# Kernel tuning notes

Hardware: AMD Instinct MI355X
Metric: run time of the kernel (lower is better)

## Reference

```python
import jax, jax.numpy as jnp
import numpy as np

N = 50000      # nodes
E = 800000     # edges (avg degree 16)
D_IN = 64
H = 128        # capacity
LAT = 64       # latent_dim
LN_EPS = 1e-5


def setup_inputs() -> dict:
    key = jax.random.key(0)
    ks = jax.random.split(key, 16)
    inp = {}
    inp["x"] = jax.random.normal(ks[0], (N, D_IN), dtype=jnp.float32)
    inp["edge_index"] = jax.random.randint(ks[1], (2, E), 0, N)
    dims = [(D_IN, H), (H, H), (H, LAT)]
    ki = 2
    for t in ("m", "v"):  # mu tower / logvar tower
        for i, (di, do) in enumerate(dims):
            s = 1.0 / np.sqrt(di)
            inp[f"{t}Wl{i}"] = jax.random.normal(ks[ki], (do, di), jnp.float32) * s; ki += 1
            inp[f"{t}bl{i}"] = jnp.zeros((do,), jnp.float32)
            inp[f"{t}Wr{i}"] = jax.random.normal(ks[ki], (do, di), jnp.float32) * s; ki += 1
            if i < 2:  # LayerNorm on hidden layers only
                inp[f"{t}g{i}"] = jnp.ones((do,), jnp.float32)
                inp[f"{t}b{i}"] = jnp.zeros((do,), jnp.float32)
    return inp


def _ln(h, g, b):
    m = h.mean(-1, keepdims=True)
    v = h.var(-1, keepdims=True)
    return (h - m) * jax.lax.rsqrt(v + LN_EPS) * g + b


def _sage(h, src, dst, inv_deg, Wl, bl, Wr):
    # mean neighbor aggregation: scatter-add messages h[src] into dst, divide by degree
    agg = jax.ops.segment_sum(h[src], dst, num_segments=N) * inv_deg  # [N, d_in]
    # PyG SAGEConv: lin_l(agg) [with bias] + lin_r(h_root) [no bias]
    return agg @ Wl.T + bl + h @ Wr.T


def _tower(x, src, dst, inv_deg, layers):
    h = x
    L = len(layers)
    for i, lay in enumerate(layers):
        h = _sage(h, src, dst, inv_deg, lay[0], lay[1], lay[2])
        if i < L - 1:
            h = jax.nn.relu(_ln(h, lay[3], lay[4]))
    return h


def reference(x, edge_index,
              mWl0, mbl0, mWr0, mg0, mb0,
              mWl1, mbl1, mWr1, mg1, mb1,
              mWl2, mbl2, mWr2,
              vWl0, vbl0, vWr0, vg0, vb0,
              vWl1, vbl1, vWr1, vg1, vb1,
              vWl2, vbl2, vWr2):
    src, dst = edge_index[0], edge_index[1]
    deg = jax.ops.segment_sum(jnp.ones((E,), x.dtype), dst, num_segments=N)
    inv_deg = (1.0 / jnp.maximum(deg, 1.0))[:, None]
    mu_layers = [(mWl0, mbl0, mWr0, mg0, mb0),
                 (mWl1, mbl1, mWr1, mg1, mb1),
                 (mWl2, mbl2, mWr2)]
    lv_layers = [(vWl0, vbl0, vWr0, vg0, vb0),
                 (vWl1, vbl1, vWr1, vg1, vb1),
                 (vWl2, vbl2, vWr2)]
    mu = _tower(x, src, dst, inv_deg, mu_layers)
    lv = _tower(x, src, dst, inv_deg, lv_layers)
    return mu, lv
```

## Files before the change

### kernel.cpp

```cpp
#include <hip/hip_runtime.h>

#define NN 50000
#define NE 800000
#define MPAD 50048
#define NBK 196
#define FB 98
#define CH4 2048
#define EB4 200000
#define STAGE_CAP 6144

typedef __attribute__((ext_vector_type(8))) short short8;
typedef __attribute__((ext_vector_type(4))) float f32x4;
typedef uint __attribute__((ext_vector_type(4))) uintx4;
typedef uint __attribute__((ext_vector_type(2))) uintx2;
typedef int __attribute__((ext_vector_type(2))) intx2;

__device__ __forceinline__ ushort f2b(float f) {
    uint u = __builtin_bit_cast(uint, f);
    uint r = (u + 0x7fffu + ((u >> 16) & 1u)) >> 16;
    return (ushort)r;
}
__device__ __forceinline__ uint pk2(float a, float b) {
    return (uint)f2b(a) | ((uint)f2b(b) << 16);
}
__device__ __forceinline__ float blo(uint u) { return __builtin_bit_cast(float, u << 16); }
__device__ __forceinline__ float bhi(uint u) { return __builtin_bit_cast(float, u & 0xffff0000u); }

__device__ __forceinline__ void acc8(float* a, uintx4 u) {
    a[0] += blo(u[0]); a[1] += bhi(u[0]);
    a[2] += blo(u[1]); a[3] += bhi(u[1]);
    a[4] += blo(u[2]); a[5] += bhi(u[2]);
    a[6] += blo(u[3]); a[7] += bhi(u[3]);
}
__device__ __forceinline__ void acc4(float* a, uintx2 u) {
    a[0] += blo(u[0]); a[1] += bhi(u[0]);
    a[2] += blo(u[1]); a[3] += bhi(u[1]);
}


struct W2Args {
    const float* srcA[8];
    const float* srcB[8];
    ushort* dst[8];
};


struct PrepArgs {
    const float* x; ushort* xb;
    W2Args w;
    const int* edst; int* bhist;
};

__global__ __launch_bounds__(256) void k_prep(PrepArgs a) {
    __shared__ int h[NBK];
    int b = blockIdx.x;
    int t = threadIdx.x;
    if (b < FB) {
        for (int i = t; i < NBK; i += 256) h[i] = 0;
        __syncthreads();
        int i1 = min((b + 1) * CH4, EB4);
        for (int i = b * CH4 + t; i < i1; i += 256) {
            int4 d = ((const int4*)a.edst)[i];
            atomicAdd(&h[d.x >> 8], 1);
            atomicAdd(&h[d.y >> 8], 1);
            atomicAdd(&h[d.z >> 8], 1);
            atomicAdd(&h[d.w >> 8], 1);
        }
        __syncthreads();
        for (int i = t; i < NBK; i += 256) a.bhist[b * NBK + i] = h[i];
    } else if (b < FB + 512) {
        const int offT[8]   = {0, 16384, 49152, 57344, 65536, 81920, 114688, 122880};
        const int splitT[8] = {64, 128, 128, 0, 64, 128, 128, 0};
        const int logKKT[8] = {7, 8, 7, 7, 7, 8, 7, 7};
        const int ntT[8]    = {8, 8, 4, 4, 8, 8, 4, 4};
        int idx = (b - FB) * 256 + t;
        if (idx >= 131072) return;
        int L = 0;
#pragma unroll
        for (int i = 1; i < 8; ++i) if (idx >= offT[i]) L = i;
        int j = idx - offT[L];
        int lk = logKKT[L];
        int KK = 1 << lk;
        int n = j >> lk;
        int c = j & (KK - 1);
        int split = splitT[L];
        float v = (c < split) ? a.w.srcA[L][n * split + c]
                              : a.w.srcB[L][n * (KK - split) + (c - split)];
        int ks = c >> 5, kseg = (c >> 3) & 3, jj = c & 7;
        int nt = n >> 4, r15 = n & 15;
        int lane = (kseg << 4) | r15;
        int foff = ((ks * ntT[L] + nt) << 9) + (lane << 3) + jj;
        a.w.dst[L][foff] = f2b(v);
    } else {
        int i = (b - FB - 512) * 256 + t;
        if (i < NN * 32) {
            float2 v = *(const float2*)(a.x + (size_t)i * 2);
            *(uint*)(a.xb + (size_t)i * 2) = pk2(v.x, v.y);
        }
    }
}


__global__ __launch_bounds__(256) void k_fscan(const int* __restrict__ bhist,
                                               int* __restrict__ pairRel,
                                               int* __restrict__ bbase) {
    __shared__ int tot[256];
    int b = threadIdx.x;
    int run = 0;
    if (b < NBK) {
        for (int blk = 0; blk < FB; ++blk) {
            int v = bhist[blk * NBK + b];
            pairRel[blk * NBK + b] = run;
            run += v;
        }
    }
    tot[b] = (b < NBK) ? run : 0;
    __syncthreads();
    for (int off = 1; off < 256; off <<= 1) {
        int t = (b >= off) ? tot[b - off] : 0;
        __syncthreads();
        tot[b] += t;
        __syncthreads();
    }
    if (b < NBK) bbase[b] = tot[b] - run;
    if (b == NBK - 1) bbase[NBK] = tot[b];
}

__global__ __launch_bounds__(256) void k_f2(const int* __restrict__ src, const int* __restrict__ dst,
                                            const int* __restrict__ pairRel,
                                            const int* __restrict__ bbase, intx2* __restrict__ pairs) {
    __shared__ int cur[NBK];
    for (int i = threadIdx.x; i < NBK; i += 256)
        cur[i] = bbase[i] + pairRel[blockIdx.x * NBK + i];
    __syncthreads();
    int i1 = min((int)(blockIdx.x + 1) * CH4, EB4);
    for (int i = blockIdx.x * CH4 + threadIdx.x; i < i1; i += 256) {
        int4 s = ((const int4*)src)[i];
        int4 d = ((const int4*)dst)[i];
        int p0 = atomicAdd(&cur[d.x >> 8], 1);
        int p1 = atomicAdd(&cur[d.y >> 8], 1);
        int p2 = atomicAdd(&cur[d.z >> 8], 1);
        int p3 = atomicAdd(&cur[d.w >> 8], 1);
        __builtin_nontemporal_store((intx2){s.x, d.x}, &pairs[p0]);
        __builtin_nontemporal_store((intx2){s.y, d.y}, &pairs[p1]);
        __builtin_nontemporal_store((intx2){s.z, d.z}, &pairs[p2]);
        __builtin_nontemporal_store((intx2){s.w, d.w}, &pairs[p3]);
    }
}

__global__ __launch_bounds__(256) void k_f3(const intx2* __restrict__ pairs,
                                            const int* __restrict__ bbase,
                                            int* __restrict__ row_start,
                                            float* __restrict__ inv_deg,
                                            int* __restrict__ col) {
    __shared__ int ndeg[256];
    __shared__ int noff[256];
    __shared__ int stage[STAGE_CAP];
    int b = blockIdx.x;
    int base = bbase[b], end = bbase[b + 1];
    int nbase = b << 8;
    int t = threadIdx.x;
    ndeg[t] = 0;
    __syncthreads();
    for (int p = base + t; p < end; p += 256) {
        intx2 pr = pairs[p];
        atomicAdd(&ndeg[pr[1] - nbase], 1);
    }
    __syncthreads();
    int d = ndeg[t];
    noff[t] = d;
    __syncthreads();
    for (int off = 1; off < 256; off <<= 1) {
        int v = (t >= off) ? noff[t - off] : 0;
        __syncthreads();
        noff[t] += v;
        __syncthreads();
    }
    int excl = noff[t] - d;
    int node = nbase + t;
    if (node < NN) {
        row_start[node] = base + excl;
        inv_deg[node] = 1.0f / (float)(d > 1 ? d : 1);
    }
    if (b == 0 && t == 0) row_start[NN] = NE;
    __syncthreads();
    noff[t] = excl;
    __syncthreads();
    int cnt = end - base;
    for (int p = base + t; p < end; p += 256) {
        intx2 pr = pairs[p];
        int pos = atomicAdd(&noff[pr[1] - nbase], 1);
        if (pos < STAGE_CAP) stage[pos] = pr[0];
        else col[base + pos] = pr[0];
    }
    __syncthreads();
    int lim = cnt < STAGE_CAP ? cnt : STAGE_CAP;
    for (int i = t; i < lim; i += 256) col[base + i] = stage[i];
}


template <int D>
__global__ __launch_bounds__(256) void k_agg(
    const ushort* __restrict__ h,
    const int* __restrict__ row_start, const int* __restrict__ col,
    const float* __restrict__ inv_deg, ushort* __restrict__ o) {
    constexpr int LPN = (D == 256) ? 32 : 16;
    int gid = blockIdx.x * 256 + threadIdx.x;
    int node = gid / LPN;
    int li = gid & (LPN - 1);
    if (node >= NN) return;
    int s = row_start[node], e = row_start[node + 1];
    float sc = inv_deg[node];
    if (D == 64) {
        const ushort* hb = h + li * 4;
        float a[4] = {0, 0, 0, 0};
        int p = s;
        for (; p + 15 < e; p += 16) {
            int cc[16];
#pragma unroll
            for (int j = 0; j < 16; ++j) cc[j] = __builtin_nontemporal_load(col + p + j);
#pragma unroll
            for (int j = 0; j < 16; ++j) acc4(a, *(const uintx2*)(hb + (size_t)cc[j] * 64));
        }
        for (; p + 3 < e; p += 4) {
            int cc[4];
#pragma unroll
            for (int j = 0; j < 4; ++j) cc[j] = __builtin_nontemporal_load(col + p + j);
#pragma unroll
            for (int j = 0; j < 4; ++j) acc4(a, *(const uintx2*)(hb + (size_t)cc[j] * 64));
        }
        for (; p < e; ++p) acc4(a, *(const uintx2*)(hb + (size_t)col[p] * 64));
        uintx2 r;
        r[0] = pk2(a[0] * sc, a[1] * sc);
        r[1] = pk2(a[2] * sc, a[3] * sc);
        __builtin_nontemporal_store(r, (uintx2*)(o + (size_t)node * 64 + li * 4));
    } else {
        const ushort* hb = h + li * 8;
        float a[8] = {0, 0, 0, 0, 0, 0, 0, 0};
        int p = s;
        for (; p + 15 < e; p += 16) {
            int cc[16];
#pragma unroll
            for (int j = 0; j < 16; ++j) cc[j] = __builtin_nontemporal_load(col + p + j);
#pragma unroll
            for (int j = 0; j < 16; ++j) acc8(a, *(const uintx4*)(hb + (size_t)cc[j] * D));
        }
        for (; p + 3 < e; p += 4) {
            int cc[4];
#pragma unroll
            for (int j = 0; j < 4; ++j) cc[j] = __builtin_nontemporal_load(col + p + j);
#pragma unroll
            for (int j = 0; j < 4; ++j) acc8(a, *(const uintx4*)(hb + (size_t)cc[j] * D));
        }
        for (; p < e; ++p) acc8(a, *(const uintx4*)(hb + (size_t)col[p] * D));
        uintx4 r;
        r[0] = pk2(a[0] * sc, a[1] * sc);
        r[1] = pk2(a[2] * sc, a[3] * sc);
        r[2] = pk2(a[4] * sc, a[5] * sc);
        r[3] = pk2(a[6] * sc, a[7] * sc);
        __builtin_nontemporal_store(r, (uintx4*)(o + (size_t)node * D + li * 8));
    }
}


struct GArgs {
    const ushort *A1, *A2, *Wm, *Wv;
    const float *blm, *blv, *gm, *gv, *bbm, *bbv;
    void* out;
};

template <int KH, int NOUT, bool DO_LN, bool DUAL, int ASTR, int AOFFM, int OSTR, int OOFFM>
__global__ __launch_bounds__(256, 2) void k_gemm(GArgs a) {
    constexpr int NT = NOUT / 16;
    constexpr int NK = KH / 16;
    constexpr int TW = DUAL ? 2 : 1;
    constexpr int WCH = NOUT * KH * 4 / 16;
    __shared__ uint4 wlds[TW * WCH];

    int tid = threadIdx.x;
    int lane = tid & 63, wid = tid >> 6;
    int tow = DUAL ? 0 : blockIdx.y;
    int aoff = tow * AOFFM;

    {
        const uint4* w0 = (const uint4*)(tow ? a.Wv : a.Wm);
        for (int i = tid; i < WCH; i += 256) wlds[i] = w0[i];
        if (DUAL) {
            const uint4* w1 = (const uint4*)a.Wv;
            for (int i = tid; i < WCH; i += 256) wlds[WCH + i] = w1[i];
        }
    }

    int r15 = lane & 15, kseg = lane >> 4;
    int m0 = blockIdx.x * 128 + wid * 32;
    size_t ar0 = (size_t)(m0 + r15);
    size_t ar1 = (size_t)(m0 + 16 + r15);

    short8 af[2][NK];
#pragma unroll
    for (int ks = 0; ks < NK; ++ks) {
        int kc = ks * 32 + kseg * 8;
        af[0][ks] = (kc < KH) ? *(const short8*)(a.A1 + ar0 * ASTR + aoff + kc)
                              : *(const short8*)(a.A2 + ar0 * ASTR + aoff + (kc - KH));
        af[1][ks] = (kc < KH) ? *(const short8*)(a.A1 + ar1 * ASTR + aoff + kc)
                              : *(const short8*)(a.A2 + ar1 * ASTR + aoff + (kc - KH));
    }
    __syncthreads();

    f32x4 acc[TW][2][NT];
#pragma unroll
    for (int tt = 0; tt < TW; ++tt)
#pragma unroll
        for (int t = 0; t < 2; ++t)
#pragma unroll
            for (int nt = 0; nt < NT; ++nt) acc[tt][t][nt] = (f32x4){0.f, 0.f, 0.f, 0.f};

#pragma unroll
    for (int ks = 0; ks < NK; ++ks) {
#pragma unroll
        for (int nt = 0; nt < NT; ++nt) {
#pragma unroll
            for (int tt = 0; tt < TW; ++tt) {
                short8 w = *(const short8*)&wlds[tt * WCH + (ks * NT + nt) * 64 + lane];
                acc[tt][0][nt] = __builtin_amdgcn_mfma_f32_16x16x32_bf16(af[0][ks], w, acc[tt][0][nt], 0, 0, 0);
                acc[tt][1][nt] = __builtin_amdgcn_mfma_f32_16x16x32_bf16(af[1][ks], w, acc[tt][1][nt], 0, 0, 0);
            }
        }
    }

#pragma unroll
    for (int tt = 0; tt < TW; ++tt) {
        int tsel = DUAL ? tt : tow;
        int ooff = tsel * OOFFM;
        const float* bl = tsel ? a.blv : a.blm;
#pragma unroll
        for (int nt = 0; nt < NT; ++nt) {
            float bb = bl[nt * 16 + r15];
#pragma unroll
            for (int t = 0; t < 2; ++t)
#pragma unroll
                for (int r = 0; r < 4; ++r) acc[tt][t][nt][r] += bb;
        }
        if (DO_LN) {
            const float* g = tsel ? a.gv : a.gm;
            const float* b = tsel ? a.bbv : a.bbm;
#pragma unroll
            for (int t = 0; t < 2; ++t) {
                float s[4] = {0, 0, 0, 0}, q[4] = {0, 0, 0, 0};
#pragma unroll
                for (int nt = 0; nt < NT; ++nt)
#pragma unroll
                    for (int r = 0; r < 4; ++r) { float v = acc[tt][t][nt][r]; s[r] += v; q[r] += v * v; }
#pragma unroll
                for (int off = 1; off < 16; off <<= 1)
#pragma unroll
                    for (int r = 0; r < 4; ++r) { s[r] += __shfl_xor(s[r], off); q[r] += __shfl_xor(q[r], off); }
                float mean[4], rstd[4];
#pragma unroll
                for (int r = 0; r < 4; ++r) {
                    mean[r] = s[r] * (1.0f / NOUT);
                    float var = q[r] * (1.0f / NOUT) - mean[r] * mean[r];
                    rstd[r] = rsqrtf(var + 1e-5f);
                }
                ushort* out = (ushort*)a.out;
#pragma unroll
                for (int nt = 0; nt < NT; ++nt) {
                    int n = nt * 16 + r15;
                    float gg = g[n], bb = b[n];
#pragma unroll
                    for (int r = 0; r < 4; ++r) {
                        int row = m0 + t * 16 + kseg * 4 + r;
                        if (row < NN) {
                            float y = fmaxf((acc[tt][t][nt][r] - mean[r]) * rstd[r] * gg + bb, 0.0f);
                            out[(size_t)row * OSTR + ooff + n] = f2b(y);
                        }
                    }
                }
            }
        } else {
            float* out = (float*)a.out;
#pragma unroll
            for (int t = 0; t < 2; ++t)
#pragma unroll
                for (int nt = 0; nt < NT; ++nt) {
                    int n = nt * 16 + r15;
#pragma unroll
                    for (int r = 0; r < 4; ++r) {
                        int row = m0 + t * 16 + kseg * 4 + r;
                        if (row < NN) out[(size_t)row * OSTR + ooff + n] = acc[tt][t][nt][r];
                    }
                }
        }
    }
}


struct G2Args {
    const ushort *A, *Wm, *Wv, *a2;
    const float *blm, *blv;
    void *outm, *outv;
};

template <bool FINAL>
__global__ __launch_bounds__(256, 2) void k_gemm2(G2Args a) {
    constexpr int NT = 4, NK = 4;
    constexpr int WCH = 1024;
    __shared__ uint4 wlds[WCH];

    int tid = threadIdx.x;
    int lane = tid & 63, wid = tid >> 6;
    int tow = blockIdx.y;
    {
        const uint4* w0 = (const uint4*)(tow ? a.Wv : a.Wm);
        for (int i = tid; i < WCH; i += 256) wlds[i] = w0[i];
    }
    int r15 = lane & 15, kseg = lane >> 4;
    int m0 = blockIdx.x * 128 + wid * 32;
    size_t ar0 = (size_t)(m0 + r15);
    size_t ar1 = (size_t)(m0 + 16 + r15);
    int aoff = tow * 128;

    short8 af[2][NK];
#pragma unroll
    for (int ks = 0; ks < NK; ++ks) {
        int kc = ks * 32 + kseg * 8;
        af[0][ks] = *(const short8*)(a.A + ar0 * 256 + aoff + kc);
        af[1][ks] = *(const short8*)(a.A + ar1 * 256 + aoff + kc);
    }
    __syncthreads();

    f32x4 acc[2][NT];
#pragma unroll
    for (int t = 0; t < 2; ++t)
#pragma unroll
        for (int nt = 0; nt < NT; ++nt) acc[t][nt] = (f32x4){0.f, 0.f, 0.f, 0.f};

#pragma unroll
    for (int ks = 0; ks < NK; ++ks) {
#pragma unroll
        for (int nt = 0; nt < NT; ++nt) {
            short8 w = *(const short8*)&wlds[(ks * NT + nt) * 64 + lane];
            acc[0][nt] = __builtin_amdgcn_mfma_f32_16x16x32_bf16(af[0][ks], w, acc[0][nt], 0, 0, 0);
            acc[1][nt] = __builtin_amdgcn_mfma_f32_16x16x32_bf16(af[1][ks], w, acc[1][nt], 0, 0, 0);
        }
    }

    if (FINAL) {
        const float* bl = tow ? a.blv : a.blm;
        float* out = (float*)(tow ? a.outv : a.outm);
#pragma unroll
        for (int t = 0; t < 2; ++t)
#pragma unroll
            for (int nt = 0; nt < NT; ++nt) {
                int n = nt * 16 + r15;
                float bb = bl[n];
#pragma unroll
                for (int r = 0; r < 4; ++r) {
                    int row = m0 + t * 16 + kseg * 4 + r;
                    if (row < NN) {
                        float av = blo((uint)a.a2[(size_t)row * 128 + tow * 64 + n]);
                        out[(size_t)row * 64 + n] = acc[t][nt][r] + bb + av;
                    }
                }
            }
    } else {
        ushort* out = (ushort*)a.outm;
#pragma unroll
        for (int t = 0; t < 2; ++t)
#pragma unroll
            for (int nt = 0; nt < NT; ++nt) {
                int n = nt * 16 + r15;
#pragma unroll
                for (int r = 0; r < 4; ++r) {
                    int row = m0 + t * 16 + kseg * 4 + r;
                    if (row < NN) out[(size_t)row * 128 + tow * 64 + n] = f2b(acc[t][nt][r]);
                }
            }
    }
}


extern "C" void kernel_launch(void* const* d_in, const int* in_sizes, int n_in,
                              void* d_out, int out_size, void* d_ws, size_t ws_size,
                              hipStream_t stream) {
    const float* x = (const float*)d_in[0];
    const int* ei = (const int*)d_in[1];
    const int* esrc = ei;
    const int* edst = ei + NE;

    const float* mWl0 = (const float*)d_in[2];
    const float* mbl0 = (const float*)d_in[3];
    const float* mWr0 = (const float*)d_in[4];
    const float* mg0  = (const float*)d_in[5];
    const float* mb0  = (const float*)d_in[6];
    const float* mWl1 = (const float*)d_in[7];
    const float* mbl1 = (const float*)d_in[8];
    const float* mWr1 = (const float*)d_in[9];
    const float* mg1  = (const float*)d_in[10];
    const float* mb1  = (const float*)d_in[11];
    const float* mWl2 = (const float*)d_in[12];
    const float* mbl2 = (const float*)d_in[13];
    const float* mWr2 = (const float*)d_in[14];
    const float* vWl0 = (const float*)d_in[15];
    const float* vbl0 = (const float*)d_in[16];
    const float* vWr0 = (const float*)d_in[17];
    const float* vg0  = (const float*)d_in[18];
    const float* vb0  = (const float*)d_in[19];
    const float* vWl1 = (const float*)d_in[20];
    const float* vbl1 = (const float*)d_in[21];
    const float* vWr1 = (const float*)d_in[22];
    const float* vg1  = (const float*)d_in[23];
    const float* vb1  = (const float*)d_in[24];
    const float* vWl2 = (const float*)d_in[25];
    const float* vbl2 = (const float*)d_in[26];
    const float* vWr2 = (const float*)d_in[27];

    char* p = (char*)d_ws;
    auto alloc = [&](size_t bytes) {
        void* r = (void*)p;
        p += (bytes + 255) & ~(size_t)255;
        return r;
    };
    int* bhist     = (int*)alloc((size_t)FB * NBK * 4);
    int* pairRel   = (int*)alloc((size_t)FB * NBK * 4);
    int* bbase     = (int*)alloc((size_t)(NBK + 1) * 4);
    int* row_start = (int*)alloc((size_t)(NN + 1) * 4);
    float* inv_deg = (float*)alloc((size_t)NN * 4);
    int* col       = (int*)alloc((size_t)NE * 4);
    intx2* pairs   = (intx2*)alloc((size_t)NE * 8);
    ushort* agg0   = (ushort*)pairs;
    ushort* x_bf   = (ushort*)alloc((size_t)MPAD * 64 * 2);
    ushort* h1p    = (ushort*)alloc((size_t)MPAD * 256 * 2);
    ushort* h2p    = (ushort*)alloc((size_t)MPAD * 256 * 2);
    ushort* aggp   = (ushort*)alloc((size_t)MPAD * 256 * 2);
    ushort* p2     = aggp;
    ushort* a2     = aggp + (size_t)MPAD * 128;
    ushort* wc0    = (ushort*)alloc((size_t)128 * 128 * 2);
    ushort* wc1    = (ushort*)alloc((size_t)128 * 256 * 2);
    ushort* wc2    = (ushort*)alloc((size_t)64 * 128 * 2);
    ushort* wc3    = (ushort*)alloc((size_t)128 * 128 * 2);
    ushort* wc4    = (ushort*)alloc((size_t)128 * 256 * 2);
    ushort* wc5    = (ushort*)alloc((size_t)64 * 128 * 2);
    ushort* wc6    = (ushort*)alloc((size_t)64 * 128 * 2);
    ushort* wc7    = (ushort*)alloc((size_t)64 * 128 * 2);

    float* out_mu = (float*)d_out;
    float* out_lv = (float*)d_out + (size_t)NN * 64;

    PrepArgs pa;
    pa.x = x; pa.xb = x_bf; pa.edst = edst; pa.bhist = bhist;
    pa.w.srcA[0] = mWl0; pa.w.srcB[0] = mWr0; pa.w.dst[0] = wc0;
    pa.w.srcA[1] = mWl1; pa.w.srcB[1] = mWr1; pa.w.dst[1] = wc1;
    pa.w.srcA[2] = mWl2; pa.w.srcB[2] = nullptr; pa.w.dst[2] = wc2;
    pa.w.srcA[3] = nullptr; pa.w.srcB[3] = mWr2; pa.w.dst[3] = wc6;
    pa.w.srcA[4] = vWl0; pa.w.srcB[4] = vWr0; pa.w.dst[4] = wc3;
    pa.w.srcA[5] = vWl1; pa.w.srcB[5] = vWr1; pa.w.dst[5] = wc4;
    pa.w.srcA[6] = vWl2; pa.w.srcB[6] = nullptr; pa.w.dst[6] = wc5;
    pa.w.srcA[7] = nullptr; pa.w.srcB[7] = vWr2; pa.w.dst[7] = wc7;
    k_prep<<<FB + 512 + (NN * 32 + 255) / 256, 256, 0, stream>>>(pa);

    k_fscan<<<1, 256, 0, stream>>>(bhist, pairRel, bbase);
    k_f2<<<FB, 256, 0, stream>>>(esrc, edst, pairRel, bbase, pairs);
    k_f3<<<NBK, 256, 0, stream>>>(pairs, bbase, row_start, inv_deg, col);

    const int gM = MPAD / 128;

    k_agg<64><<<(NN * 16 + 255) / 256, 256, 0, stream>>>(x_bf, row_start, col, inv_deg, agg0);
    {
        GArgs ga = {agg0, x_bf, wc0, wc3, mbl0, vbl0, mg0, vg0, mb0, vb0, h1p};
        k_gemm<64, 128, true, true, 64, 0, 256, 128><<<dim3(gM, 1), 256, 0, stream>>>(ga);
    }
    k_agg<256><<<(NN * 32 + 255) / 256, 256, 0, stream>>>(h1p, row_start, col, inv_deg, aggp);
    {
        GArgs ga = {aggp, h1p, wc1, wc4, mbl1, vbl1, mg1, vg1, mb1, vb1, h2p};
        k_gemm<128, 128, true, false, 256, 128, 256, 128><<<dim3(gM, 2), 256, 0, stream>>>(ga);
    }
    {
        G2Args g2 = {h2p, wc2, wc5, nullptr, nullptr, nullptr, p2, nullptr};
        k_gemm2<false><<<dim3(gM, 2), 256, 0, stream>>>(g2);
    }
    k_agg<128><<<(NN * 16 + 255) / 256, 256, 0, stream>>>(p2, row_start, col, inv_deg, a2);
    {
        G2Args g2 = {h2p, wc6, wc7, a2, mbl2, vbl2, out_mu, out_lv};
        k_gemm2<true><<<dim3(gM, 2), 256, 0, stream>>>(g2);
    }
}
```

Baseline: 375.5 us.

## Gather hidden features in 8-bit float format for the neighbor aggregation passes

The first GEMM now also writes an 8-bit float copy of h1, and the projection GEMM writes its output p2 in a signed 8-bit float format. The layer-1 and layer-2 neighbor gathers read these byte-wide rows and decode them in registers, which halves the bytes moved by the bandwidth-bound random gathers. The cost is a large loss of precision (a 7-bit exponent/mantissa encoding with a scale), which may break the accuracy tolerance, plus extra encode and decode arithmetic. Unroll depth drops from 16 to 8 and nontemporal stores are replaced with normal stores.

Result: faster. 352.6 us (-6.1%).

```diff
diff --git a/kernel.cpp b/kernel.cpp
--- a/kernel.cpp
+++ b/kernel.cpp
@@ -13,7 +13,6 @@
 typedef __attribute__((ext_vector_type(4))) float f32x4;
 typedef uint __attribute__((ext_vector_type(4))) uintx4;
 typedef uint __attribute__((ext_vector_type(2))) uintx2;
-typedef int __attribute__((ext_vector_type(2))) intx2;
 
 __device__ __forceinline__ ushort f2b(float f) {
     uint u = __builtin_bit_cast(uint, f);
@@ -25,6 +24,16 @@
 }
 __device__ __forceinline__ float blo(uint u) { return __builtin_bit_cast(float, u << 16); }
 __device__ __forceinline__ float bhi(uint u) { return __builtin_bit_cast(float, u & 0xffff0000u); }
+
+__device__ __forceinline__ uint enc8u(float y) {
+    uint b = __builtin_bit_cast(uint, y * 0x1p-120f) + (1u << 19);
+    return (b >> 20) & 0x7fu;
+}
+__device__ __forceinline__ uint enc8s(float y) {
+    uint sb = __builtin_bit_cast(uint, y) & 0x80000000u;
+    uint b = __builtin_bit_cast(uint, fabsf(y) * 0x1p-120f) + (1u << 19);
+    return ((b >> 20) & 0x7fu) | (sb >> 24);
+}
 
 __device__ __forceinline__ void acc8(float* a, uintx4 u) {
     a[0] += blo(u[0]); a[1] += bhi(u[0]);
@@ -35,6 +44,19 @@
 __device__ __forceinline__ void acc4(float* a, uintx2 u) {
     a[0] += blo(u[0]); a[1] += bhi(u[0]);
     a[2] += blo(u[1]); a[3] += bhi(u[1]);
+}
+template <bool SIGNED>
+__device__ __forceinline__ void accf8(float* a, uintx2 u, float c120) {
+#pragma unroll
+    for (int w = 0; w < 2; ++w) {
+        uint v = u[w];
+#pragma unroll
+        for (int j = 0; j < 4; ++j) {
+            uint b = (v >> (8 * j)) & 0xffu;
+            uint f = SIGNED ? (((b & 0x80u) << 24) | ((b & 0x7fu) << 20)) : (b << 20);
+            a[w * 4 + j] += __builtin_bit_cast(float, f) * c120;
+        }
+    }
 }
 
 
@@ -128,7 +150,7 @@
 
 __global__ __launch_bounds__(256) void k_f2(const int* __restrict__ src, const int* __restrict__ dst,
                                             const int* __restrict__ pairRel,
-                                            const int* __restrict__ bbase, intx2* __restrict__ pairs) {
+                                            const int* __restrict__ bbase, int2* __restrict__ pairs) {
     __shared__ int cur[NBK];
     for (int i = threadIdx.x; i < NBK; i += 256)
         cur[i] = bbase[i] + pairRel[blockIdx.x * NBK + i];
@@ -141,14 +163,14 @@
         int p1 = atomicAdd(&cur[d.y >> 8], 1);
         int p2 = atomicAdd(&cur[d.z >> 8], 1);
         int p3 = atomicAdd(&cur[d.w >> 8], 1);
-        __builtin_nontemporal_store((intx2){s.x, d.x}, &pairs[p0]);
-        __builtin_nontemporal_store((intx2){s.y, d.y}, &pairs[p1]);
-        __builtin_nontemporal_store((intx2){s.z, d.z}, &pairs[p2]);
-        __builtin_nontemporal_store((intx2){s.w, d.w}, &pairs[p3]);
-    }
-}
-
-__global__ __launch_bounds__(256) void k_f3(const intx2* __restrict__ pairs,
+        pairs[p0] = (int2){s.x, d.x};
+        pairs[p1] = (int2){s.y, d.y};
+        pairs[p2] = (int2){s.z, d.z};
+        pairs[p3] = (int2){s.w, d.w};
+    }
+}
+
+__global__ __launch_bounds__(256) void k_f3(const int2* __restrict__ pairs,
                                             const int* __restrict__ bbase,
                                             int* __restrict__ row_start,
                                             float* __restrict__ inv_deg,
@@ -162,10 +184,7 @@
     int t = threadIdx.x;
     ndeg[t] = 0;
     __syncthreads();
-    for (int p = base + t; p < end; p += 256) {
-        intx2 pr = pairs[p];
-        atomicAdd(&ndeg[pr[1] - nbase], 1);
-    }
+    for (int p = base + t; p < end; p += 256) atomicAdd(&ndeg[pairs[p].y - nbase], 1);
     __syncthreads();
     int d = ndeg[t];
     noff[t] = d;
@@ -188,10 +207,10 @@
     __syncthreads();
     int cnt = end - base;
     for (int p = base + t; p < end; p += 256) {
-        intx2 pr = pairs[p];
-        int pos = atomicAdd(&noff[pr[1] - nbase], 1);
-        if (pos < STAGE_CAP) stage[pos] = pr[0];
-        else col[base + pos] = pr[0];
+        int2 pr = pairs[p];
+        int pos = atomicAdd(&noff[pr.y - nbase], 1);
+        if (pos < STAGE_CAP) stage[pos] = pr.x;
+        else col[base + pos] = pr.x;
     }
     __syncthreads();
     int lim = cnt < STAGE_CAP ? cnt : STAGE_CAP;
@@ -199,67 +218,64 @@
 }
 
 
-template <int D>
-__global__ __launch_bounds__(256) void k_agg(
+__global__ __launch_bounds__(256) void k_agg64(
     const ushort* __restrict__ h,
     const int* __restrict__ row_start, const int* __restrict__ col,
     const float* __restrict__ inv_deg, ushort* __restrict__ o) {
-    constexpr int LPN = (D == 256) ? 32 : 16;
+    int gid = blockIdx.x * 256 + threadIdx.x;
+    int node = gid >> 4;
+    int li = gid & 15;
+    if (node >= NN) return;
+    int s = row_start[node], e = row_start[node + 1];
+    float sc = inv_deg[node];
+    const ushort* hb = h + li * 4;
+    float a[4] = {0, 0, 0, 0};
+    int p = s;
+    for (; p + 7 < e; p += 8) {
+        int cc[8];
+#pragma unroll
+        for (int j = 0; j < 8; ++j) cc[j] = __builtin_nontemporal_load(col + p + j);
+#pragma unroll
+        for (int j = 0; j < 8; ++j) acc4(a, *(const uintx2*)(hb + (size_t)cc[j] * 64));
+    }
+    for (; p < e; ++p) acc4(a, *(const uintx2*)(hb + (size_t)col[p] * 64));
+    uintx2 r;
+    r[0] = pk2(a[0] * sc, a[1] * sc);
+    r[1] = pk2(a[2] * sc, a[3] * sc);
+    *(uintx2*)(o + (size_t)node * 64 + li * 4) = r;
+}
+
+
+template <int D, bool SIGNED>
+__global__ __launch_bounds__(256) void k_agg8(
+    const uchar* __restrict__ h,
+    const int* __restrict__ row_start, const int* __restrict__ col,
+    const float* __restrict__ inv_deg, ushort* __restrict__ o) {
+    constexpr int LPN = D / 8;
     int gid = blockIdx.x * 256 + threadIdx.x;
     int node = gid / LPN;
     int li = gid & (LPN - 1);
     if (node >= NN) return;
     int s = row_start[node], e = row_start[node + 1];
     float sc = inv_deg[node];
-    if (D == 64) {
-        const ushort* hb = h + li * 4;
-        float a[4] = {0, 0, 0, 0};
-        int p = s;
-        for (; p + 15 < e; p += 16) {
-            int cc[16];
-#pragma unroll
-            for (int j = 0; j < 16; ++j) cc[j] = __builtin_nontemporal_load(col + p + j);
-#pragma unroll
-            for (int j = 0; j < 16; ++j) acc4(a, *(const uintx2*)(hb + (size_t)cc[j] * 64));
-        }
-        for (; p + 3 < e; p += 4) {
-            int cc[4];
-#pragma unroll
-            for (int j = 0; j < 4; ++j) cc[j] = __builtin_nontemporal_load(col + p + j);
-#pragma unroll
-            for (int j = 0; j < 4; ++j) acc4(a, *(const uintx2*)(hb + (size_t)cc[j] * 64));
-        }
-        for (; p < e; ++p) acc4(a, *(const uintx2*)(hb + (size_t)col[p] * 64));
-        uintx2 r;
-        r[0] = pk2(a[0] * sc, a[1] * sc);
-        r[1] = pk2(a[2] * sc, a[3] * sc);
-        __builtin_nontemporal_store(r, (uintx2*)(o + (size_t)node * 64 + li * 4));
-    } else {
-        const ushort* hb = h + li * 8;
-        float a[8] = {0, 0, 0, 0, 0, 0, 0, 0};
-        int p = s;
-        for (; p + 15 < e; p += 16) {
-            int cc[16];
-#pragma unroll
-            for (int j = 0; j < 16; ++j) cc[j] = __builtin_nontemporal_load(col + p + j);
-#pragma unroll
-            for (int j = 0; j < 16; ++j) acc8(a, *(const uintx4*)(hb + (size_t)cc[j] * D));
-        }
-        for (; p + 3 < e; p += 4) {
-            int cc[4];
-#pragma unroll
-            for (int j = 0; j < 4; ++j) cc[j] = __builtin_nontemporal_load(col + p + j);
-#pragma unroll
-            for (int j = 0; j < 4; ++j) acc8(a, *(const uintx4*)(hb + (size_t)cc[j] * D));
-        }
-        for (; p < e; ++p) acc8(a, *(const uintx4*)(hb + (size_t)col[p] * D));
-        uintx4 r;
-        r[0] = pk2(a[0] * sc, a[1] * sc);
-        r[1] = pk2(a[2] * sc, a[3] * sc);
-        r[2] = pk2(a[4] * sc, a[5] * sc);
-        r[3] = pk2(a[6] * sc, a[7] * sc);
-        __builtin_nontemporal_store(r, (uintx4*)(o + (size_t)node * D + li * 8));
-    }
+    const uchar* hb = h + li * 8;
+    const float c120 = 0x1p120f;
+    float a[8] = {0, 0, 0, 0, 0, 0, 0, 0};
+    int p = s;
+    for (; p + 7 < e; p += 8) {
+        int cc[8];
+#pragma unroll
+        for (int j = 0; j < 8; ++j) cc[j] = __builtin_nontemporal_load(col + p + j);
+#pragma unroll
+        for (int j = 0; j < 8; ++j) accf8<SIGNED>(a, *(const uintx2*)(hb + (size_t)cc[j] * D), c120);
+    }
+    for (; p < e; ++p) accf8<SIGNED>(a, *(const uintx2*)(hb + (size_t)col[p] * D), c120);
+    uintx4 r;
+    r[0] = pk2(a[0] * sc, a[1] * sc);
+    r[1] = pk2(a[2] * sc, a[3] * sc);
+    r[2] = pk2(a[4] * sc, a[5] * sc);
+    r[3] = pk2(a[6] * sc, a[7] * sc);
+    *(uintx4*)(o + (size_t)node * D + li * 8) = r;
 }
 
 
@@ -267,9 +283,10 @@
     const ushort *A1, *A2, *Wm, *Wv;
     const float *blm, *blv, *gm, *gv, *bbm, *bbv;
     void* out;
+    uchar* out8;
 };
 
-template <int KH, int NOUT, bool DO_LN, bool DUAL, int ASTR, int AOFFM, int OSTR, int OOFFM>
+template <int KH, int NOUT, bool DO_LN, bool DUAL, int ASTR, int AOFFM, int OSTR, int OOFFM, bool F8OUT>
 __global__ __launch_bounds__(256, 2) void k_gemm(GArgs a) {
     constexpr int NT = NOUT / 16;
     constexpr int NK = KH / 16;
@@ -373,6 +390,7 @@
                         if (row < NN) {
                             float y = fmaxf((acc[tt][t][nt][r] - mean[r]) * rstd[r] * gg + bb, 0.0f);
                             out[(size_t)row * OSTR + ooff + n] = f2b(y);
+                            if (F8OUT) a.out8[(size_t)row * OSTR + ooff + n] = (uchar)enc8u(y);
                         }
                     }
                 }
@@ -464,7 +482,7 @@
                 }
             }
     } else {
-        ushort* out = (ushort*)a.outm;
+        uchar* out = (uchar*)a.outm;
 #pragma unroll
         for (int t = 0; t < 2; ++t)
 #pragma unroll
@@ -473,7 +491,7 @@
 #pragma unroll
                 for (int r = 0; r < 4; ++r) {
                     int row = m0 + t * 16 + kseg * 4 + r;
-                    if (row < NN) out[(size_t)row * 128 + tow * 64 + n] = f2b(acc[t][nt][r]);
+                    if (row < NN) out[(size_t)row * 128 + tow * 64 + n] = (uchar)enc8s(acc[t][nt][r]);
                 }
             }
     }
@@ -527,13 +545,14 @@
     int* row_start = (int*)alloc((size_t)(NN + 1) * 4);
     float* inv_deg = (float*)alloc((size_t)NN * 4);
     int* col       = (int*)alloc((size_t)NE * 4);
-    intx2* pairs   = (intx2*)alloc((size_t)NE * 8);
+    int2* pairs    = (int2*)alloc((size_t)NE * 8);
     ushort* agg0   = (ushort*)pairs;
     ushort* x_bf   = (ushort*)alloc((size_t)MPAD * 64 * 2);
     ushort* h1p    = (ushort*)alloc((size_t)MPAD * 256 * 2);
     ushort* h2p    = (ushort*)alloc((size_t)MPAD * 256 * 2);
     ushort* aggp   = (ushort*)alloc((size_t)MPAD * 256 * 2);
-    ushort* p2     = aggp;
+    uchar* h1f8    = (uchar*)h2p;
+    uchar* p2f8    = (uchar*)aggp;
     ushort* a2     = aggp + (size_t)MPAD * 128;
     ushort* wc0    = (ushort*)alloc((size_t)128 * 128 * 2);
     ushort* wc1    = (ushort*)alloc((size_t)128 * 256 * 2);
@@ -565,21 +584,21 @@
 
     const int gM = MPAD / 128;
 
-    k_agg<64><<<(NN * 16 + 255) / 256, 256, 0, stream>>>(x_bf, row_start, col, inv_deg, agg0);
+    k_agg64<<<(NN * 16 + 255) / 256, 256, 0, stream>>>(x_bf, row_start, col, inv_deg, agg0);
     {
-        GArgs ga = {agg0, x_bf, wc0, wc3, mbl0, vbl0, mg0, vg0, mb0, vb0, h1p};
-        k_gemm<64, 128, true, true, 64, 0, 256, 128><<<dim3(gM, 1), 256, 0, stream>>>(ga);
-    }
-    k_agg<256><<<(NN * 32 + 255) / 256, 256, 0, stream>>>(h1p, row_start, col, inv_deg, aggp);
+        GArgs ga = {agg0, x_bf, wc0, wc3, mbl0, vbl0, mg0, vg0, mb0, vb0, h1p, h1f8};
+        k_gemm<64, 128, true, true, 64, 0, 256, 128, true><<<dim3(gM, 1), 256, 0, stream>>>(ga);
+    }
+    k_agg8<256, false><<<(NN * 32 + 255) / 256, 256, 0, stream>>>(h1f8, row_start, col, inv_deg, aggp);
     {
-        GArgs ga = {aggp, h1p, wc1, wc4, mbl1, vbl1, mg1, vg1, mb1, vb1, h2p};
-        k_gemm<128, 128, true, false, 256, 128, 256, 128><<<dim3(gM, 2), 256, 0, stream>>>(ga);
+        GArgs ga = {aggp, h1p, wc1, wc4, mbl1, vbl1, mg1, vg1, mb1, vb1, h2p, nullptr};
+        k_gemm<128, 128, true, false, 256, 128, 256, 128, false><<<dim3(gM, 2), 256, 0, stream>>>(ga);
     }
     {
-        G2Args g2 = {h2p, wc2, wc5, nullptr, nullptr, nullptr, p2, nullptr};
+        G2Args g2 = {h2p, wc2, wc5, nullptr, nullptr, nullptr, p2f8, nullptr};
         k_gemm2<false><<<dim3(gM, 2), 256, 0, stream>>>(g2);
     }
-    k_agg<128><<<(NN * 16 + 255) / 256, 256, 0, stream>>>(p2, row_start, col, inv_deg, a2);
+    k_agg8<128, true><<<(NN * 16 + 255) / 256, 256, 0, stream>>>(p2f8, row_start, col, inv_deg, a2);
     {
         G2Args g2 = {h2p, wc6, wc7, a2, mbl2, vbl2, out_mu, out_lv};
         k_gemm2<true><<<dim3(gM, 2), 256, 0, stream>>>(g2);
```
